# Kernel optimization log

Measured on AMD Instinct MI355X. Metric: run time of the kernel, lower is better.

## Reference

```python
import jax, jax.numpy as jnp
import numpy as np

B, L, H = 2, 64, 64
VOCAB = 32000
HEADS = 8
HPH = H // HEADS  # harmonics per head


def setup_inputs() -> dict:
    key = jax.random.key(0)
    ks = jax.random.split(key, 6)
    freqs = jax.random.normal(ks[0], (B, L, H), dtype=jnp.float32)
    amps = jax.random.normal(ks[1], (B, L, H), dtype=jnp.float32)
    phases = jax.random.normal(ks[2], (B, L, H), dtype=jnp.float32)
    vocab_patterns = jax.random.normal(ks[3], (VOCAB, HEADS, HPH), dtype=jnp.float32)
    # nn.Parameter init is zeros; use small noise so gradients/paths are nontrivial
    interference_phases = 0.1 * jax.random.normal(ks[4], (HEADS, HPH), dtype=jnp.float32)
    # nn.Linear(num_heads, 1): weight (1, heads), bias (1,)
    W = jax.random.normal(ks[5], (1, HEADS), dtype=jnp.float32) / np.sqrt(HEADS)
    b = jnp.zeros((1,), dtype=jnp.float32)
    return {"freqs": freqs, "amps": amps, "phases": phases,
            "vocab_patterns": vocab_patterns,
            "interference_phases": interference_phases,
            "W": W, "b": b}


def reference(freqs, amps, phases, vocab_patterns, interference_phases, W, b):
    Bb, Ll, Hh = freqs.shape
    heads = vocab_patterns.shape[1]
    hph = Hh // heads
    f = freqs.reshape(Bb, Ll, heads, hph)
    a = amps.reshape(Bb, Ll, heads, hph)
    p = phases.reshape(Bb, Ll, heads, hph)
    # phase_alignment has no vocab dependence: fold amp * cos(phase diff) first
    c = a * jnp.cos(p - interference_phases[None, None, :, :])  # (B,L,heads,hph)
    scores = []
    for h in range(heads):  # small fixed loop over heads (avoids (B,L,heads,V,hph) blowup)
        f_h = f[:, :, h, :]                      # (B,L,hph)
        vf = vocab_patterns[:, h, :]             # (V,hph)
        fm = jnp.exp(-jnp.abs(f_h[:, :, None, :] - vf[None, None, :, :]))  # (B,L,V,hph)
        scores.append(jnp.einsum('blk,blvk->blv', c[:, :, h, :], fm))
    s = jnp.stack(scores, axis=-1)               # (B,L,V,heads)
    logits = jnp.einsum('blvh,oh->blvo', s, W)[..., 0] + b[0]  # (B,L,V)
    return logits
```

## Files before the change

### kernel.cpp

```cpp
#include <hip/hip_runtime.h>
#include <math.h>

#define VOCAB   32000
#define BLTOT   128
#define HTOT    64
#define BLT     8
#define VPB     256
#define VT      2
#define SLICE   (VPB * VT)
#define NSLICE  64
#define NBLG    (BLTOT / BLT)

#define PREP1_BLOCKS 32
#define PREP2_BLOCKS ((VOCAB * 2 + 255) / 256)

#define LOG2E   1.44269504088896340736f

typedef __fp16 h2 __attribute__((ext_vector_type(2)));

__global__ void prep_fused(const float* __restrict__ freqs,
                           const float* __restrict__ amps,
                           const float* __restrict__ phases,
                           const float* __restrict__ ip,
                           const float* __restrict__ W,
                           const float4* __restrict__ vp4,
                           void* __restrict__ ws) {
    if (blockIdx.x < PREP1_BLOCKS) {
        int t = blockIdx.x * blockDim.x + threadIdx.x;
        int bl = t >> 6;
        int j  = t & 63;
        float fe = freqs[t] * LOG2E;
        float cw = amps[t] * cosf(phases[t] - ip[j]) * W[j >> 3];
        int jj = j >> 2, u = j & 3;
        __fp16* pA = (__fp16*)ws;
        __fp16* pC = (__fp16*)((char*)ws + 32768);
        int ia = (bl * 16 + jj) * 8;
        pA[ia + u]     = (__fp16)__builtin_amdgcn_exp2f(fe);
        pA[ia + 4 + u] = (__fp16)__builtin_amdgcn_exp2f(-fe);
        pC[(bl * 16 + jj) * 4 + u] = (__fp16)cw;
    } else {
        int t = (blockIdx.x - PREP1_BLOCKS) * blockDim.x + threadIdx.x;
        if (t >= VOCAB * 2) return;
        int v   = t >> 1;
        int jj0 = (t & 1) * 8;
        float4* evt4 = (float4*)((char*)ws + 49152);
#pragma unroll
        for (int l = 0; l < 8; ++l) {
            int jj = jj0 + l;
            const float4 vf = vp4[v * 16 + jj];
            float ax = vf.x * LOG2E, ay = vf.y * LOG2E;
            float az = vf.z * LOG2E, aw = vf.w * LOG2E;
            h2 ev01  = __builtin_amdgcn_cvt_pkrtz(__builtin_amdgcn_exp2f( ax),
                                                  __builtin_amdgcn_exp2f( ay));
            h2 ev23  = __builtin_amdgcn_cvt_pkrtz(__builtin_amdgcn_exp2f( az),
                                                  __builtin_amdgcn_exp2f( aw));
            h2 emv01 = __builtin_amdgcn_cvt_pkrtz(__builtin_amdgcn_exp2f(-ax),
                                                  __builtin_amdgcn_exp2f(-ay));
            h2 emv23 = __builtin_amdgcn_cvt_pkrtz(__builtin_amdgcn_exp2f(-az),
                                                  __builtin_amdgcn_exp2f(-aw));
            float4 o;
            o.x = __builtin_bit_cast(float, ev01);
            o.y = __builtin_bit_cast(float, ev23);
            o.z = __builtin_bit_cast(float, emv01);
            o.w = __builtin_bit_cast(float, emv23);
            evt4[jj * VOCAB + v] = o;
        }
    }
}

__global__ __launch_bounds__(VPB, 4) void
wave_main(const float4* __restrict__ evt4,
          const void* __restrict__ uni,
          const float* __restrict__ bptr,
          float* __restrict__ out) {
    const int tid = threadIdx.x;
    const int bid = blockIdx.x;
    const int xcd = bid & 7;
    const int j   = bid >> 3;
    const int slice = xcd + ((j >> 4) << 3);
    const int blg   = j & 15;
    const int bl0   = blg * BLT;
    const int v0    = slice * SLICE + tid;

    if (slice * SLICE >= VOCAB) return;

    const float4* gA = (const float4*)((const char*)uni + (size_t)bl0 * 256);
    const float2* gC = (const float2*)((const char*)uni + 32768 + (size_t)bl0 * 128);

    int vidx[VT];
#pragma unroll
    for (int k = 0; k < VT; ++k) {
        int v = v0 + k * VPB;
        vidx[k] = v < VOCAB ? v : VOCAB - 1;
    }

    float acc[BLT][VT];
#pragma unroll
    for (int i = 0; i < BLT; ++i)
#pragma unroll
        for (int k = 0; k < VT; ++k) acc[i][k] = 0.0f;

#pragma unroll 2
    for (int jj = 0; jj < 16; ++jj) {
        h2 evA[VT], evB[VT], emvA[VT], emvB[VT];
#pragma unroll
        for (int k = 0; k < VT; ++k) {
            const float4 E = evt4[jj * VOCAB + vidx[k]];
            evA[k]  = __builtin_bit_cast(h2, E.x);
            evB[k]  = __builtin_bit_cast(h2, E.y);
            emvA[k] = __builtin_bit_cast(h2, E.z);
            emvB[k] = __builtin_bit_cast(h2, E.w);
        }
#pragma unroll
        for (int i = 0; i < BLT; ++i) {
            const float4 A = gA[i * 16 + jj];
            const float2 C = gC[i * 16 + jj];
            const h2 ef01 = __builtin_bit_cast(h2, A.x);
            const h2 ef23 = __builtin_bit_cast(h2, A.y);
            const h2 em01 = __builtin_bit_cast(h2, A.z);
            const h2 em23 = __builtin_bit_cast(h2, A.w);
            const h2 cw01 = __builtin_bit_cast(h2, C.x);
            const h2 cw23 = __builtin_bit_cast(h2, C.y);
#pragma unroll
            for (int k = 0; k < VT; ++k) {
                h2 m01 = __builtin_elementwise_min(ef01 * emvA[k], em01 * evA[k]);
                h2 m23 = __builtin_elementwise_min(ef23 * emvB[k], em23 * evB[k]);
                acc[i][k] = __builtin_amdgcn_fdot2(m01, cw01, acc[i][k], false);
                acc[i][k] = __builtin_amdgcn_fdot2(m23, cw23, acc[i][k], false);
            }
        }
    }

    const float b0 = bptr[0];
#pragma unroll
    for (int i = 0; i < BLT; ++i)
#pragma unroll
        for (int k = 0; k < VT; ++k) {
            int v = v0 + k * VPB;
            if (v < VOCAB)
                out[(bl0 + i) * VOCAB + v] = acc[i][k] + b0;
        }
}

extern "C" void kernel_launch(void* const* d_in, const int* in_sizes, int n_in,
                              void* d_out, int out_size, void* d_ws, size_t ws_size,
                              hipStream_t stream) {
    const float* freqs  = (const float*)d_in[0];
    const float* amps   = (const float*)d_in[1];
    const float* phases = (const float*)d_in[2];
    const float* vp     = (const float*)d_in[3];
    const float* ip     = (const float*)d_in[4];
    const float* W      = (const float*)d_in[5];
    const float* b      = (const float*)d_in[6];
    float* out = (float*)d_out;

    prep_fused<<<dim3(PREP1_BLOCKS + PREP2_BLOCKS), dim3(256), 0, stream>>>(
        freqs, amps, phases, ip, W, (const float4*)vp, d_ws);

    float4* evt4 = (float4*)((char*)d_ws + 49152);
    wave_main<<<dim3(NBLG * NSLICE), dim3(VPB), 0, stream>>>(
        evt4, d_ws, b, out);
}
```

Before: 102.0 us.

## Interleave per-row prep records and prefetch next vocab slice in main loop

The per-row exp/cw tables now go into one 32-byte record per (jj, bl), so the main kernel reads them contiguously through a single pointer per jj, with padding in the cw part. The vocab exp table is moved to a larger offset. The main loop software-prefetches the next jj's vocab float4 into registers while computing the current one, to hide global load latency. This costs extra registers under launch_bounds(256,4) and a redundant final prefetch.

Result: no change. 103.4 us (+1.5%).

```diff
diff --git a/kernel.cpp b/kernel.cpp
--- a/kernel.cpp
+++ b/kernel.cpp
@@ -10,6 +10,8 @@
 #define SLICE   (VPB * VT)
 #define NSLICE  64
 #define NBLG    (BLTOT / BLT)
+
+#define EVT_OFF 65536
 
 #define PREP1_BLOCKS 32
 #define PREP2_BLOCKS ((VOCAB * 2 + 255) / 256)
@@ -32,18 +34,16 @@
         float fe = freqs[t] * LOG2E;
         float cw = amps[t] * cosf(phases[t] - ip[j]) * W[j >> 3];
         int jj = j >> 2, u = j & 3;
-        __fp16* pA = (__fp16*)ws;
-        __fp16* pC = (__fp16*)((char*)ws + 32768);
-        int ia = (bl * 16 + jj) * 8;
-        pA[ia + u]     = (__fp16)__builtin_amdgcn_exp2f(fe);
-        pA[ia + 4 + u] = (__fp16)__builtin_amdgcn_exp2f(-fe);
-        pC[(bl * 16 + jj) * 4 + u] = (__fp16)cw;
+        __fp16* rec = (__fp16*)((char*)ws + (size_t)(jj * 128 + bl) * 32);
+        rec[u]     = (__fp16)__builtin_amdgcn_exp2f(fe);
+        rec[4 + u] = (__fp16)__builtin_amdgcn_exp2f(-fe);
+        rec[8 + u] = (__fp16)cw;
     } else {
         int t = (blockIdx.x - PREP1_BLOCKS) * blockDim.x + threadIdx.x;
         if (t >= VOCAB * 2) return;
         int v   = t >> 1;
         int jj0 = (t & 1) * 8;
-        float4* evt4 = (float4*)((char*)ws + 49152);
+        float4* evt4 = (float4*)((char*)ws + EVT_OFF);
 #pragma unroll
         for (int l = 0; l < 8; ++l) {
             int jj = jj0 + l;
@@ -84,8 +84,7 @@
 
     if (slice * SLICE >= VOCAB) return;
 
-    const float4* gA = (const float4*)((const char*)uni + (size_t)bl0 * 256);
-    const float2* gC = (const float2*)((const char*)uni + 32768 + (size_t)bl0 * 128);
+    const char* fb = (const char*)uni;
 
     int vidx[VT];
 #pragma unroll
@@ -100,27 +99,37 @@
 #pragma unroll
         for (int k = 0; k < VT; ++k) acc[i][k] = 0.0f;
 
+    float4 Ecur[VT];
+#pragma unroll
+    for (int k = 0; k < VT; ++k) Ecur[k] = evt4[vidx[k]];
+
 #pragma unroll 2
     for (int jj = 0; jj < 16; ++jj) {
+        const int jn = jj < 15 ? jj + 1 : 15;
+        float4 Enext[VT];
+#pragma unroll
+        for (int k = 0; k < VT; ++k) Enext[k] = evt4[jn * VOCAB + vidx[k]];
+
+        const float4* R = (const float4*)(fb + (size_t)(jj * 128 + bl0) * 32);
+
         h2 evA[VT], evB[VT], emvA[VT], emvB[VT];
 #pragma unroll
         for (int k = 0; k < VT; ++k) {
-            const float4 E = evt4[jj * VOCAB + vidx[k]];
-            evA[k]  = __builtin_bit_cast(h2, E.x);
-            evB[k]  = __builtin_bit_cast(h2, E.y);
-            emvA[k] = __builtin_bit_cast(h2, E.z);
-            emvB[k] = __builtin_bit_cast(h2, E.w);
+            evA[k]  = __builtin_bit_cast(h2, Ecur[k].x);
+            evB[k]  = __builtin_bit_cast(h2, Ecur[k].y);
+            emvA[k] = __builtin_bit_cast(h2, Ecur[k].z);
+            emvB[k] = __builtin_bit_cast(h2, Ecur[k].w);
         }
 #pragma unroll
         for (int i = 0; i < BLT; ++i) {
-            const float4 A = gA[i * 16 + jj];
-            const float2 C = gC[i * 16 + jj];
+            const float4 A  = R[2 * i];
+            const float4 Cc = R[2 * i + 1];
             const h2 ef01 = __builtin_bit_cast(h2, A.x);
             const h2 ef23 = __builtin_bit_cast(h2, A.y);
             const h2 em01 = __builtin_bit_cast(h2, A.z);
             const h2 em23 = __builtin_bit_cast(h2, A.w);
-            const h2 cw01 = __builtin_bit_cast(h2, C.x);
-            const h2 cw23 = __builtin_bit_cast(h2, C.y);
+            const h2 cw01 = __builtin_bit_cast(h2, Cc.x);
+            const h2 cw23 = __builtin_bit_cast(h2, Cc.y);
 #pragma unroll
             for (int k = 0; k < VT; ++k) {
                 h2 m01 = __builtin_elementwise_min(ef01 * emvA[k], em01 * evA[k]);
@@ -129,6 +138,8 @@
                 acc[i][k] = __builtin_amdgcn_fdot2(m23, cw23, acc[i][k], false);
             }
         }
+#pragma unroll
+        for (int k = 0; k < VT; ++k) Ecur[k] = Enext[k];
     }
 
     const float b0 = bptr[0];
@@ -157,7 +168,7 @@
     prep_fused<<<dim3(PREP1_BLOCKS + PREP2_BLOCKS), dim3(256), 0, stream>>>(
         freqs, amps, phases, ip, W, (const float4*)vp, d_ws);
 
-    float4* evt4 = (float4*)((char*)d_ws + 49152);
+    float4* evt4 = (float4*)((char*)d_ws + EVT_OFF);
     wave_main<<<dim3(NBLG * NSLICE), dim3(VPB), 0, stream>>>(
         evt4, d_ws, b, out);
 }
```
